# Kernel optimization log

Hardware: AMD Instinct MI355X
Metric: run time of the kernel (lower is better)

## Reference

```python
import jax, jax.numpy as jnp
import numpy as np

P, B, FEAT, HID, ATTN, NHEAD = 4096, 32, 512, 512, 512, 8
HD = ATTN // NHEAD  # 64


def setup_inputs() -> dict:
    key = jax.random.key(0)
    ks = jax.random.split(key, 12)
    s = lambda n: 1.0 / np.sqrt(n)
    return {
        "last_hidden": jax.random.normal(ks[0], (1, B, HID), jnp.float32),
        "encoder_outputs": jax.random.normal(ks[1], (P, B, FEAT), jnp.float32),
        # outer projections (stored [in, out]; torch Linear is x @ W.T + b)
        "Wa_w": jax.random.uniform(ks[2], (FEAT, ATTN), jnp.float32, -s(FEAT), s(FEAT)),
        "Wa_b": jax.random.uniform(ks[3], (ATTN,), jnp.float32, -s(FEAT), s(FEAT)),
        "Ua_w": jax.random.uniform(ks[4], (HID, ATTN), jnp.float32, -s(HID), s(HID)),
        "Ua_b": jax.random.uniform(ks[5], (ATTN,), jnp.float32, -s(HID), s(HID)),
        # inner Attention(head_attn_size, head_attn_size, head_attn_size)
        "Wa2_w": jax.random.uniform(ks[6], (HD, HD), jnp.float32, -s(HD), s(HD)),
        "Wa2_b": jax.random.uniform(ks[7], (HD,), jnp.float32, -s(HD), s(HD)),
        "Ua2_w": jax.random.uniform(ks[8], (HD, HD), jnp.float32, -s(HD), s(HD)),
        "Ua2_b": jax.random.uniform(ks[9], (HD,), jnp.float32, -s(HD), s(HD)),
        "va_w": jax.random.uniform(ks[10], (HD, 1), jnp.float32, -s(HD), s(HD)),
        "va_b": jax.random.uniform(ks[11], (1,), jnp.float32, -s(HD), s(HD)),
        "nhead": NHEAD,
    }


def reference(last_hidden, encoder_outputs, Wa_w, Wa_b, Ua_w, Ua_b,
              Wa2_w, Wa2_b, Ua2_w, Ua2_b, va_w, va_b, nhead):
    p, b = encoder_outputs.shape[:2]
    enc = encoder_outputs @ Wa_w + Wa_b            # [P,B,A]
    hid = last_hidden @ Ua_w + Ua_b                # [1,B,A]
    hd = enc.shape[-1] // nhead
    enc = enc.reshape(p, b, nhead, hd)             # [P,B,nh,hd]
    hid = hid.reshape(1, b, nhead, hd)             # [1,B,nh,hd]
    # inner Bahdanau attention
    a = jnp.tanh((enc @ Wa2_w + Wa2_b) + (hid @ Ua2_w + Ua2_b))
    scores = a @ va_w + va_b                       # [P,B,nh,1]
    weights = jax.nn.softmax(scores, axis=0)       # softmax over pixels
    context = jnp.sum(weights * enc, axis=0, keepdims=True)  # [1,B,nh,hd]
    weight = jnp.mean(weights, axis=-2)            # mean over heads -> [P,B,1]
    context = context.reshape(1, b, nhead * hd)    # [1,B,A]
    return context, weight
```

## Files before the change

### kernel.cpp

```cpp
#include <hip/hip_runtime.h>
#include <hip/hip_bf16.h>

#define PDIM 4096
#define BDIM 32
#define MDIM (PDIM*BDIM)
#define KDIM 512
#define NDIM 512
#define NH   8
#define HD   64

typedef __attribute__((ext_vector_type(4))) float f32x4;
typedef __attribute__((ext_vector_type(8))) short bf16x8;

__device__ __forceinline__ unsigned short f2bf(float f) {
  unsigned u = __float_as_uint(f);
  u += 0x7fffu + ((u >> 16) & 1u);
  return (unsigned short)(u >> 16);
}
__device__ __forceinline__ float bf2f(unsigned short u) {
  return __uint_as_float(((unsigned)u) << 16);
}

__device__ __forceinline__ float fast_tanh(float x) {
  x = fminf(fmaxf(x, -15.f), 15.f);
  float e = __expf(2.f * x);
  return __fdividef(e - 1.f, e + 1.f);
}

#define GLOAD_LDS16(g, l) __builtin_amdgcn_global_load_lds( \
    (const __attribute__((address_space(1))) void*)(g),     \
    (__attribute__((address_space(3))) void*)(l), 16, 0, 0)

__global__ __launch_bounds__(256) void cvt_k(
    const float* __restrict__ x, unsigned short* __restrict__ xbf) {
  size_t i = ((size_t)blockIdx.x * 256 + threadIdx.x) * 8;
  float4 a = *(const float4*)(x + i);
  float4 b = *(const float4*)(x + i + 4);
  ushort4 o0; o0.x = f2bf(a.x); o0.y = f2bf(a.y); o0.z = f2bf(a.z); o0.w = f2bf(a.w);
  ushort4 o1; o1.x = f2bf(b.x); o1.y = f2bf(b.y); o1.z = f2bf(b.z); o1.w = f2bf(b.w);
  *(ushort4*)(xbf + i) = o0;
  *(ushort4*)(xbf + i + 4) = o1;
}

__global__ __launch_bounds__(512) void hub_k(
    const float* __restrict__ lh, const float* __restrict__ Ua,
    const float* __restrict__ Ua_b, const float* __restrict__ Ua2,
    const float* __restrict__ Ua2_b, const float* __restrict__ Wa_b,
    const float* __restrict__ Wa2, const float* __restrict__ Wa2_b,
    float* __restrict__ ubf) {
  int b = blockIdx.x, tid = threadIdx.x;
  __shared__ float ls[512];
  __shared__ float hs[512];
  ls[tid] = lh[b*512 + tid];
  __syncthreads();
  float s = Ua_b[tid];
  #pragma unroll 8
  for (int k = 0; k < 512; ++k)
    s += ls[k] * Ua[(size_t)k*512 + tid];
  hs[tid] = s;
  __syncthreads();
  int h = tid >> 6, j = tid & 63;
  float u = Ua2_b[j] + Wa2_b[j];
  #pragma unroll 4
  for (int k = 0; k < 64; ++k) {
    u += hs[h*64 + k] * Ua2[k*64 + j];
    u += Wa_b[h*64 + k] * Wa2[k*64 + j];
  }
  ubf[b*512 + tid] = u;
}

__global__ __launch_bounds__(256) void wft_k(
    const float* __restrict__ Wa, const float* __restrict__ Wa2,
    unsigned short* __restrict__ WfT) {
  int n = blockIdx.x, tid = threadIdx.x;
  int h = n >> 6, j = n & 63;
  __shared__ float w2[64];
  if (tid < 64) w2[tid] = Wa2[tid*64 + j];
  __syncthreads();
  for (int k = tid; k < 512; k += 256) {
    float s = 0.f;
    #pragma unroll 8
    for (int kk = 0; kk < 64; ++kk)
      s += Wa[(size_t)k*512 + h*64 + kk] * w2[kk];
    WfT[(size_t)n*512 + k] = f2bf(s);
  }
}

__global__ __launch_bounds__(256, 2) void gemm_score_k(
    const unsigned short* __restrict__ xbf, const unsigned short* __restrict__ WfT,
    const float* __restrict__ ubf, const float* __restrict__ va_w,
    const float* __restrict__ va_b, float* __restrict__ scores) {
  __shared__ __align__(16) unsigned short As[2][8192];
  __shared__ __align__(16) unsigned short Bs[2][8192];
  int tid = threadIdx.x;
  int orig = blockIdx.x;
  int wg = (orig & 7) * 512 + (orig >> 3);
  int bn = wg & 3, bm = wg >> 2;
  int m0 = bm*128, n0 = bn*128;
  int lane = tid & 63, w = tid >> 6;
  int quad = lane >> 4, l16 = lane & 15;
  int wr = w >> 1, wc = w & 1;
  f32x4 acc[4][4] = {};

  #pragma unroll
  for (int i = 0; i < 4; ++i) {
    int c = i*256 + tid;
    int r = c & 127, kc = c >> 7;
    GLOAD_LDS16(xbf + (size_t)(m0 + r)*512 + kc*8, &As[0][(size_t)c*8]);
  }
  #pragma unroll
  for (int i = 0; i < 4; ++i) {
    int c = i*256 + tid;
    int r = c & 127, kc = c >> 7;
    GLOAD_LDS16(WfT + (size_t)(n0 + r)*512 + kc*8, &Bs[0][(size_t)c*8]);
  }
  __syncthreads();

  #pragma unroll
  for (int t = 0; t < 8; ++t) {
    int cur = t & 1, nxt = cur ^ 1;
    if (t < 7) {
      int kn = (t + 1) * 64;
      #pragma unroll
      for (int i = 0; i < 4; ++i) {
        int c = i*256 + tid;
        int r = c & 127, kc = c >> 7;
        GLOAD_LDS16(xbf + (size_t)(m0 + r)*512 + kn + kc*8, &As[nxt][(size_t)c*8]);
      }
      #pragma unroll
      for (int i = 0; i < 4; ++i) {
        int c = i*256 + tid;
        int r = c & 127, kc = c >> 7;
        GLOAD_LDS16(WfT + (size_t)(n0 + r)*512 + kn + kc*8, &Bs[nxt][(size_t)c*8]);
      }
    }
    const unsigned short* Ab = &As[cur][0];
    const unsigned short* Bb = &Bs[cur][0];
    #pragma unroll
    for (int kk = 0; kk < 64; kk += 32) {
      int kc = (kk >> 3) + quad;
      bf16x8 af[4], bfr[4];
      #pragma unroll
      for (int ti = 0; ti < 4; ++ti)
        af[ti] = *(const bf16x8*)(Ab + ((size_t)kc*128 + 64*wr + 16*ti + l16)*8);
      #pragma unroll
      for (int tj = 0; tj < 4; ++tj)
        bfr[tj] = *(const bf16x8*)(Bb + ((size_t)kc*128 + 64*wc + 16*tj + l16)*8);
      #pragma unroll
      for (int ti = 0; ti < 4; ++ti)
        #pragma unroll
        for (int tj = 0; tj < 4; ++tj)
          acc[ti][tj] = __builtin_amdgcn_mfma_f32_16x16x32_bf16(
              af[ti], bfr[tj], acc[ti][tj], 0, 0, 0);
    }
    __syncthreads();
  }

  float* ubf_s = (float*)&As[0][0];
  #pragma unroll
  for (int t = 0; t < 16; ++t) {
    int idx = t*256 + tid;
    int b = idx >> 7, c = idx & 127;
    ubf_s[b*129 + c] = ubf[b*512 + n0 + c];
  }
  __syncthreads();

  int head = bn*2 + wc;
  float va_r[4];
  #pragma unroll
  for (int tj = 0; tj < 4; ++tj) va_r[tj] = va_w[16*tj + l16];
  float vb = va_b[0];
  #pragma unroll
  for (int ti = 0; ti < 4; ++ti) {
    #pragma unroll
    for (int r = 0; r < 4; ++r) {
      int row_loc = 64*wr + 16*ti + 4*quad + r;
      int b31 = row_loc & 31;
      float s = 0.f;
      #pragma unroll
      for (int tj = 0; tj < 4; ++tj) {
        float xa = acc[ti][tj][r] + ubf_s[b31*129 + 64*wc + 16*tj + l16];
        s += fast_tanh(xa) * va_r[tj];
      }
      s += __shfl_xor(s, 1); s += __shfl_xor(s, 2);
      s += __shfl_xor(s, 4); s += __shfl_xor(s, 8);
      if (l16 == 0) {
        int m = m0 + row_loc;
        scores[((size_t)head*32 + (m & 31))*4096 + (m >> 5)] = s + vb;
      }
    }
  }
}

__global__ __launch_bounds__(256) void softmax_k(
    const float* __restrict__ sc, float* __restrict__ w) {
  int bh = blockIdx.x;
  int tid = threadIdx.x;
  const float* row = sc + (size_t)bh*4096;
  float4 v[4];
  float mx = -1e30f;
  #pragma unroll
  for (int i = 0; i < 4; ++i) {
    v[i] = *(const float4*)(row + (size_t)(i*256 + tid)*4);
    mx = fmaxf(mx, fmaxf(fmaxf(v[i].x, v[i].y), fmaxf(v[i].z, v[i].w)));
  }
  #pragma unroll
  for (int m = 1; m < 64; m <<= 1) mx = fmaxf(mx, __shfl_xor(mx, m));
  __shared__ float redm[4], reds[4];
  int wid = tid >> 6, lane = tid & 63;
  if (lane == 0) redm[wid] = mx;
  __syncthreads();
  mx = fmaxf(fmaxf(redm[0], redm[1]), fmaxf(redm[2], redm[3]));
  float sum = 0.f;
  #pragma unroll
  for (int i = 0; i < 4; ++i) {
    v[i].x = __expf(v[i].x - mx); v[i].y = __expf(v[i].y - mx);
    v[i].z = __expf(v[i].z - mx); v[i].w = __expf(v[i].w - mx);
    sum += v[i].x + v[i].y + v[i].z + v[i].w;
  }
  #pragma unroll
  for (int m = 1; m < 64; m <<= 1) sum += __shfl_xor(sum, m);
  if (lane == 0) reds[wid] = sum;
  __syncthreads();
  sum = reds[0] + reds[1] + reds[2] + reds[3];
  float inv = 1.f / sum;
  float* dst = w + (size_t)bh*4096;
  #pragma unroll
  for (int i = 0; i < 4; ++i) {
    float4 o; o.x = v[i].x*inv; o.y = v[i].y*inv; o.z = v[i].z*inv; o.w = v[i].w*inv;
    *(float4*)(dst + (size_t)(i*256 + tid)*4) = o;
  }
}

__global__ __launch_bounds__(256) void mean_k(
    const float* __restrict__ w, float* __restrict__ out) {
  int p0 = blockIdx.x * 256;
  int tid = threadIdx.x;
  float s[32];
  #pragma unroll
  for (int b = 0; b < 32; ++b) s[b] = 0.f;
  for (int h = 0; h < 8; ++h) {
    #pragma unroll
    for (int b = 0; b < 32; ++b)
      s[b] += w[((size_t)h*32 + b)*4096 + p0 + tid];
  }
  float4* dst = (float4*)(out + BDIM*NDIM + (size_t)(p0 + tid)*32);
  #pragma unroll
  for (int j = 0; j < 8; ++j) {
    float4 o;
    o.x = s[4*j]*0.125f; o.y = s[4*j+1]*0.125f;
    o.z = s[4*j+2]*0.125f; o.w = s[4*j+3]*0.125f;
    dst[j] = o;
  }
}

__global__ __launch_bounds__(256) void ctx_partial_k(
    const unsigned short* __restrict__ xbf, const float* __restrict__ w,
    float* __restrict__ part) {
  int pc = blockIdx.x;
  int b  = blockIdx.y;
  int tid = threadIdx.x;
  __shared__ float wl[8*256];
  __shared__ float red[4][512];
  #pragma unroll
  for (int h = 0; h < 8; ++h)
    wl[h*256 + tid] = w[((size_t)h*32 + b)*4096 + pc*256 + tid];
  __syncthreads();
  int lane = tid & 63, wv = tid >> 6;
  float acc[8][8];
  #pragma unroll
  for (int h = 0; h < 8; ++h)
    #pragma unroll
    for (int j = 0; j < 8; ++j) acc[h][j] = 0.f;
  for (int i = 0; i < 64; ++i) {
    int pl = wv*64 + i;
    bf16x8 xv = *(const bf16x8*)(xbf + ((size_t)((pc*256 + pl)*32 + b))*512 + lane*8);
    float xf[8];
    #pragma unroll
    for (int j = 0; j < 8; ++j) xf[j] = bf2f((unsigned short)xv[j]);
    #pragma unroll
    for (int h = 0; h < 8; ++h) {
      float ww = wl[h*256 + pl];
      #pragma unroll
      for (int j = 0; j < 8; ++j) acc[h][j] += ww * xf[j];
    }
  }
  for (int h = 0; h < 8; ++h) {
    #pragma unroll
    for (int j = 0; j < 8; j += 4)
      *(float4*)(&red[wv][lane*8 + j]) = *(float4*)(&acc[h][j]);
    __syncthreads();
    if (tid < 64) {
      #pragma unroll
      for (int j = 0; j < 8; ++j) {
        int f = tid*8 + j;
        part[((size_t)(b*16 + pc)*NH + h)*512 + f] =
            red[0][f] + red[1][f] + red[2][f] + red[3][f];
      }
    }
    __syncthreads();
  }
}

__global__ __launch_bounds__(256) void ctx_reduce_k(
    const float* __restrict__ part, float* __restrict__ cx) {
  int gid = blockIdx.x*256 + threadIdx.x;
  float s = 0.f;
  int f = gid & 511;
  int bh = gid >> 9;
  int h = bh & 7, b = bh >> 3;
  #pragma unroll
  for (int pc = 0; pc < 16; ++pc)
    s += part[((size_t)(b*16 + pc)*NH + h)*512 + f];
  cx[gid] = s;
}

__global__ __launch_bounds__(256) void ctx_proj_k(
    const float* __restrict__ cx, const float* __restrict__ Wa,
    const float* __restrict__ Wa_b, float* __restrict__ out) {
  int b = blockIdx.x >> 3, h = blockIdx.x & 7;
  int tid = threadIdx.x;
  __shared__ float cs[512];
  cs[tid]       = cx[(size_t)blockIdx.x*512 + tid];
  cs[tid + 256] = cx[(size_t)blockIdx.x*512 + tid + 256];
  __syncthreads();
  int d = tid & 63, g = tid >> 6;
  float s = 0.f;
  #pragma unroll 8
  for (int f = g*128; f < g*128 + 128; ++f)
    s += cs[f] * Wa[(size_t)f*512 + h*64 + d];
  __shared__ float red[256];
  red[tid] = s;
  __syncthreads();
  if (tid < 64) {
    float tot = red[tid] + red[64+tid] + red[128+tid] + red[192+tid] + Wa_b[h*64 + tid];
    out[b*512 + h*64 + tid] = tot;
  }
}

extern "C" void kernel_launch(void* const* d_in, const int* in_sizes, int n_in,
                              void* d_out, int out_size, void* d_ws, size_t ws_size,
                              hipStream_t stream) {
  (void)in_sizes; (void)n_in; (void)out_size; (void)ws_size;
  const float* lh    = (const float*)d_in[0];
  const float* x     = (const float*)d_in[1];
  const float* Wa_w  = (const float*)d_in[2];
  const float* Wa_b  = (const float*)d_in[3];
  const float* Ua_w  = (const float*)d_in[4];
  const float* Ua_b  = (const float*)d_in[5];
  const float* Wa2_w = (const float*)d_in[6];
  const float* Wa2_b = (const float*)d_in[7];
  const float* Ua2_w = (const float*)d_in[8];
  const float* Ua2_b = (const float*)d_in[9];
  const float* va_w  = (const float*)d_in[10];
  const float* va_b  = (const float*)d_in[11];
  float* out = (float*)d_out;
  char* ws = (char*)d_ws;

  unsigned short* xbf = (unsigned short*)(ws);
  unsigned short* WfT = (unsigned short*)(ws + 134217728);
  float* ubf    = (float*)(ws + 134742016);
  float* scores = (float*)(ws + 134807552);
  float* w      = (float*)(ws + 139001856);
  float* part   = (float*)(ws + 143196160);
  float* cx     = (float*)(ws + 151584768);

  hipLaunchKernelGGL(cvt_k, dim3(32768), dim3(256), 0, stream, x, xbf);
  hipLaunchKernelGGL(hub_k, dim3(32), dim3(512), 0, stream,
                     lh, Ua_w, Ua_b, Ua2_w, Ua2_b, Wa_b, Wa2_w, Wa2_b, ubf);
  hipLaunchKernelGGL(wft_k, dim3(512), dim3(256), 0, stream, Wa_w, Wa2_w, WfT);
  hipLaunchKernelGGL(gemm_score_k, dim3(4096), dim3(256), 0, stream,
                     xbf, WfT, ubf, va_w, va_b, scores);
  hipLaunchKernelGGL(softmax_k, dim3(256), dim3(256), 0, stream, scores, w);
  hipLaunchKernelGGL(mean_k, dim3(16), dim3(256), 0, stream, w, out);
  hipLaunchKernelGGL(ctx_partial_k, dim3(16, 32), dim3(256), 0, stream, xbf, w, part);
  hipLaunchKernelGGL(ctx_reduce_k, dim3(512), dim3(256), 0, stream, part, cx);
  hipLaunchKernelGGL(ctx_proj_k, dim3(256), dim3(256), 0, stream, cx, Wa_w, Wa_b, out);
}
```

Measured before the change: 684.1 us.

## Single-buffer GEMM LDS tiles to fit four workgroups per CU

The score GEMM kernel drops its double-buffered LDS staging for a single 32 KB shared buffer, loading each K-slice with a sync before and after. Launch bounds rise from 2 to 4 workgroups per CU. The aim is to hide global-load latency through more resident waves rather than explicit prefetch overlap. In exchange, each block now stalls on its own loads, and the tighter register budget may cause spills given the 64-float accumulator.

```diff
diff --git a/kernel.cpp b/kernel.cpp
--- a/kernel.cpp
+++ b/kernel.cpp
@@ -86,12 +86,13 @@
   }
 }
 
-__global__ __launch_bounds__(256, 2) void gemm_score_k(
+__global__ __launch_bounds__(256, 4) void gemm_score_k(
     const unsigned short* __restrict__ xbf, const unsigned short* __restrict__ WfT,
     const float* __restrict__ ubf, const float* __restrict__ va_w,
     const float* __restrict__ va_b, float* __restrict__ scores) {
-  __shared__ __align__(16) unsigned short As[2][8192];
-  __shared__ __align__(16) unsigned short Bs[2][8192];
+  __shared__ __align__(16) unsigned short sm[16384];
+  unsigned short* As = sm;
+  unsigned short* Bs = sm + 8192;
   int tid = threadIdx.x;
   int orig = blockIdx.x;
   int wg = (orig & 7) * 512 + (orig >> 3);
@@ -102,50 +103,31 @@
   int wr = w >> 1, wc = w & 1;
   f32x4 acc[4][4] = {};
 
-  #pragma unroll
-  for (int i = 0; i < 4; ++i) {
-    int c = i*256 + tid;
-    int r = c & 127, kc = c >> 7;
-    GLOAD_LDS16(xbf + (size_t)(m0 + r)*512 + kc*8, &As[0][(size_t)c*8]);
-  }
-  #pragma unroll
-  for (int i = 0; i < 4; ++i) {
-    int c = i*256 + tid;
-    int r = c & 127, kc = c >> 7;
-    GLOAD_LDS16(WfT + (size_t)(n0 + r)*512 + kc*8, &Bs[0][(size_t)c*8]);
-  }
-  __syncthreads();
-
-  #pragma unroll
-  for (int t = 0; t < 8; ++t) {
-    int cur = t & 1, nxt = cur ^ 1;
-    if (t < 7) {
-      int kn = (t + 1) * 64;
-      #pragma unroll
-      for (int i = 0; i < 4; ++i) {
-        int c = i*256 + tid;
-        int r = c & 127, kc = c >> 7;
-        GLOAD_LDS16(xbf + (size_t)(m0 + r)*512 + kn + kc*8, &As[nxt][(size_t)c*8]);
-      }
-      #pragma unroll
-      for (int i = 0; i < 4; ++i) {
-        int c = i*256 + tid;
-        int r = c & 127, kc = c >> 7;
-        GLOAD_LDS16(WfT + (size_t)(n0 + r)*512 + kn + kc*8, &Bs[nxt][(size_t)c*8]);
-      }
-    }
-    const unsigned short* Ab = &As[cur][0];
-    const unsigned short* Bb = &Bs[cur][0];
+  for (int k0 = 0; k0 < KDIM; k0 += 64) {
+    __syncthreads();
+    #pragma unroll
+    for (int i = 0; i < 4; ++i) {
+      int c = i*256 + tid;
+      int r = c & 127, kc = c >> 7;
+      GLOAD_LDS16(xbf + (size_t)(m0 + r)*512 + k0 + kc*8, As + (size_t)c*8);
+    }
+    #pragma unroll
+    for (int i = 0; i < 4; ++i) {
+      int c = i*256 + tid;
+      int r = c & 127, kc = c >> 7;
+      GLOAD_LDS16(WfT + (size_t)(n0 + r)*512 + k0 + kc*8, Bs + (size_t)c*8);
+    }
+    __syncthreads();
     #pragma unroll
     for (int kk = 0; kk < 64; kk += 32) {
       int kc = (kk >> 3) + quad;
       bf16x8 af[4], bfr[4];
       #pragma unroll
       for (int ti = 0; ti < 4; ++ti)
-        af[ti] = *(const bf16x8*)(Ab + ((size_t)kc*128 + 64*wr + 16*ti + l16)*8);
+        af[ti] = *(const bf16x8*)(As + ((size_t)kc*128 + 64*wr + 16*ti + l16)*8);
       #pragma unroll
       for (int tj = 0; tj < 4; ++tj)
-        bfr[tj] = *(const bf16x8*)(Bb + ((size_t)kc*128 + 64*wc + 16*tj + l16)*8);
+        bfr[tj] = *(const bf16x8*)(Bs + ((size_t)kc*128 + 64*wc + 16*tj + l16)*8);
       #pragma unroll
       for (int ti = 0; ti < 4; ++ti)
         #pragma unroll
@@ -153,10 +135,10 @@
           acc[ti][tj] = __builtin_amdgcn_mfma_f32_16x16x32_bf16(
               af[ti], bfr[tj], acc[ti][tj], 0, 0, 0);
     }
-    __syncthreads();
-  }
-
-  float* ubf_s = (float*)&As[0][0];
+  }
+
+  __syncthreads();
+  float* ubf_s = (float*)sm;
   #pragma unroll
   for (int t = 0; t < 16; ++t) {
     int idx = t*256 + tid;
```

Measured after the change: 643.6 us. -5.9%, faster.
